# Performance work log

Measured on AMD Instinct MI355X. Metric: run time of the kernel, lower is better.

Reference implementation:

```python
import jax, jax.numpy as jnp
import numpy as np
from jax import lax

# 4D convolution: XLA's general conv supports 4 spatial dims directly.
# dim numbers: N C + 4 spatial (H1 W1 H2 W2)
_DN = ('NCHWDT', 'OIHWDT', 'NCHWDT')


def conv4d(x, w, b):
    # x: [B, Cin, H1, W1, H2, W2]; w: [Cout, Cin, 3,3,3,3]; b: [Cout]
    y = lax.conv_general_dilated(x, w, window_strides=(1, 1, 1, 1),
                                 padding=[(1, 1)] * 4,
                                 dimension_numbers=_DN)
    return y + b.reshape(1, -1, 1, 1, 1, 1)


def setup_inputs() -> dict:
    key = jax.random.key(0)
    ks = jax.random.split(key, 7)
    B, S = 2, 30
    x = jax.random.normal(ks[0], (B, 1, S, S, S, S), dtype=jnp.float32)
    # Conv4d weights, fan-in scaled (kernel 3^4 = 81)
    w1 = jax.random.normal(ks[1], (10, 1, 3, 3, 3, 3), dtype=jnp.float32) * (1.0 / np.sqrt(1 * 81))
    b1 = jax.random.normal(ks[2], (10,), dtype=jnp.float32) * 0.01
    w2 = jax.random.normal(ks[3], (10, 10, 3, 3, 3, 3), dtype=jnp.float32) * (1.0 / np.sqrt(10 * 81))
    b2 = jax.random.normal(ks[4], (10,), dtype=jnp.float32) * 0.01
    w3 = jax.random.normal(ks[5], (1, 10, 3, 3, 3, 3), dtype=jnp.float32) * (1.0 / np.sqrt(10 * 81))
    b3 = jax.random.normal(ks[6], (1,), dtype=jnp.float32) * 0.01
    return {"x": x, "w1": w1, "b1": b1, "w2": w2, "b2": b2, "w3": w3, "b3": b3}


def reference(x, w1, b1, w2, b2, w3, b3):
    def net(t):
        for w, b in ((w1, b1), (w2, b2), (w3, b3)):
            t = jax.nn.relu(conv4d(t, w, b))
        return t

    # symmetric mode: f(x) + permute(f(permute(x)))
    perm = (0, 1, 4, 5, 2, 3)
    return net(x) + jnp.transpose(net(jnp.transpose(x, perm)), perm)
```

## Files before the change

### kernel.cpp

```cpp
#include <hip/hip_runtime.h>


static constexpr int S  = 30;
static constexpr long S4 = 810000;
static constexpr size_t PLANE = 32768;
static constexpr size_t YBYTES = (size_t)1800 * PLANE;

typedef __bf16 bf16x8 __attribute__((ext_vector_type(8)));
typedef float  f32x16 __attribute__((ext_vector_type(16)));
typedef unsigned int  u32;
typedef unsigned short u16;

static __device__ __forceinline__ u16 f2bf(float f) {
    u32 u = __builtin_bit_cast(u32, f);
    return (u16)((u + 0x7fffu + ((u >> 16) & 1u)) >> 16);
}

__global__ __launch_bounds__(256) void fragprep_k(u32* __restrict__ ft,
    const float* __restrict__ w1, const float* __restrict__ w2,
    const float* __restrict__ w3)
{
    const int gid = blockIdx.x * 256 + threadIdx.x;
    if (gid >= 6 * 27 * 64 + 2 * 3 * 64) return;
    const int lane = gid & 63;
    const int n = lane & 31, hl = lane >> 5;
    u16 us[8];
#pragma unroll
    for (int j = 0; j < 8; ++j) us[j] = 0;

    if (gid < 6 * 27 * 64) {
        int r = gid >> 6;
        const int k3 = r % 3; r /= 3;
        const int k12 = r % 9; const int set = r / 9;
        const int layer = set >> 1, swap = set & 1;
        const int k1 = k12 / 3, k2 = k12 % 3;
        if (n < 30) {
            const int k4 = (n < 10) ? 0 : ((n < 20) ? 1 : 2);
            const int co = n - 10 * k4;
            const int i1 = swap ? k3 : k1, i2 = swap ? k4 : k2;
            const int i3 = swap ? k1 : k3, i4 = swap ? k2 : k4;
            const int widx = ((i1 * 3 + i2) * 3 + i3) * 3 + i4;
#pragma unroll
            for (int j = 0; j < 8; ++j) {
                const int k = hl * 8 + j;
                float wv = 0.f;
                if (layer == 0) { if (k == 0) wv = w1[co * 81 + widx]; }
                else if (layer == 1) { if (k < 10) wv = w2[(co * 10 + k) * 81 + widx]; }
                else { if (k < 10 && co == 0) wv = w3[k * 81 + widx]; }
                us[j] = f2bf(wv);
            }
        }
    } else {
        const int idx = gid - 6 * 27 * 64;
        int r = idx >> 6;
        const int k3 = r % 3, swap = r / 3;
        if (n < 30) {
            const int k4 = (n < 10) ? 0 : ((n < 20) ? 1 : 2);
            const int co = n - 10 * k4;
#pragma unroll
            for (int j = 0; j < 8; ++j) {
                const int k12 = hl * 8 + j;
                if (k12 < 9) {
                    const int k1 = k12 / 3, k2 = k12 % 3;
                    const int i1 = swap ? k3 : k1, i2 = swap ? k4 : k2;
                    const int i3 = swap ? k1 : k3, i4 = swap ? k2 : k4;
                    const int widx = ((i1 * 3 + i2) * 3 + i3) * 3 + i4;
                    us[j] = f2bf(w1[co * 81 + widx]);
                }
            }
        }
    }
    u32* o = ft + (size_t)gid * 4;
    o[0] = (u32)us[0] | ((u32)us[1] << 16);
    o[1] = (u32)us[2] | ((u32)us[3] << 16);
    o[2] = (u32)us[4] | ((u32)us[5] << 16);
    o[3] = (u32)us[6] | ((u32)us[7] << 16);
}

__global__ __launch_bounds__(128) void zerok(u16* __restrict__ y1, u16* __restrict__ y2)
{
    const int pb = blockIdx.x, tid = threadIdx.x;
    if (tid >= 124) return;
    int hp, tp;
    if (tid < 32)      { hp = 0;        tp = tid; }
    else if (tid < 64) { hp = 31;       tp = tid - 32; }
    else if (tid < 94) { hp = tid - 63; tp = 0; }
    else               { hp = tid - 93; tp = 31; }
    const size_t off = (size_t)pb * PLANE + hp * 1024 + tp * 32;
    const uint4 z = make_uint4(0, 0, 0, 0);
    *(uint4*)((char*)y1 + off)      = z;
    *(uint4*)((char*)y1 + off + 16) = z;
    *(uint4*)((char*)y2 + off)      = z;
    *(uint4*)((char*)y2 + off + 16) = z;
}

__global__ __launch_bounds__(256, 4) void conv0_k(
    const float* __restrict__ x, const uint4* __restrict__ bt,
    const float* __restrict__ bias, void* __restrict__ outp)
{
    __shared__ float E[4][1056];
    const int wgid = blockIdx.x + S * blockIdx.y + 900 * blockIdx.z;
    const int id2  = (wgid & 7) * 450 + (wgid >> 3);
    const int half = id2 & 1;
    int sp = id2 >> 1;
    const int w1i = sp % S; sp /= S;
    const int h1  = sp % S;
    const int b   = sp / S;

    const int tid = threadIdx.x;
    const int lane = tid & 63, wv = tid >> 6;
    const int m = lane & 31, hl = lane >> 5;
    const int rbase = half * 15 + wv * 4;

    uint4 Bs[3];
#pragma unroll
    for (int ss = 0; ss < 3; ++ss) Bs[ss] = bt[ss * 64 + lane];

    int gof[9]; int gokm = 0;
#pragma unroll
    for (int k12 = 0; k12 < 9; ++k12) {
        const int g1 = h1 + k12 / 3 - 1, g2 = w1i + k12 % 3 - 1;
        gof[k12] = 0;
        if (g1 >= 0 && g1 < S && g2 >= 0 && g2 < S) {
            gof[k12] = (g1 * S + g2) * 900; gokm |= 1 << k12;
        }
    }
    const float* xb = x + (size_t)b * S4;

    uint4 F[6];
#pragma unroll
    for (int f = 0; f < 6; ++f) {
        const int hp = rbase + f;
        const bool rk = (hp >= 1 && hp <= 30 && m >= 1 && m <= 30);
        const int ro = (hp - 1) * 30 + (m - 1);
        u16 av[8];
#pragma unroll
        for (int j = 0; j < 8; ++j) av[j] = 0;
        if (hl == 0) {
#pragma unroll
            for (int j = 0; j < 8; ++j) {
                float v = 0.f;
                if (rk && ((gokm >> j) & 1)) v = xb[gof[j] + ro];
                av[j] = f2bf(v);
            }
        } else {
            float v = 0.f;
            if (rk && ((gokm >> 8) & 1)) v = xb[gof[8] + ro];
            av[0] = f2bf(v);
        }
        F[f] = make_uint4((u32)av[0] | ((u32)av[1] << 16),
                          (u32)av[2] | ((u32)av[3] << 16),
                          (u32)av[4] | ((u32)av[5] << 16),
                          (u32)av[6] | ((u32)av[7] << 16));
    }

    f32x16 acc[4];
#pragma unroll
    for (int r = 0; r < 4; ++r)
#pragma unroll
        for (int e = 0; e < 16; ++e) acc[r][e] = 0.f;
#pragma unroll
    for (int ss = 0; ss < 3; ++ss)
#pragma unroll
        for (int r = 0; r < 4; ++r)
            acc[r] = __builtin_amdgcn_mfma_f32_32x32x16_bf16(
                __builtin_bit_cast(bf16x8, F[r + ss]),
                __builtin_bit_cast(bf16x8, Bs[ss]), acc[r], 0, 0, 0);

    float* Ew = E[wv];
    for (int r = 0; r < 4; ++r) {
        if (wv == 3 && r == 3) continue;
#pragma unroll
        for (int gq = 0; gq < 4; ++gq)
#pragma unroll
            for (int r4 = 0; r4 < 4; ++r4)
                Ew[m * 33 + 4 * hl + 8 * gq + r4] = acc[r][gq * 4 + r4];

        const int h2 = rbase + r;
        char* pl = (char*)outp + ((size_t)b * 900 + h1 * S + w1i) * PLANE
                   + (size_t)(h2 + 1) * 1024;
        const int t = lane >> 1, h8 = lane & 1;
        if (t < 30) {
            u32 wo[4];
#pragma unroll
            for (int p = 0; p < 4; ++p) {
                const int c0 = 8 * h8 + 2 * p, c1 = c0 + 1;
                float v0 = 0.f, v1 = 0.f;
                if (c0 < 10)
                    v0 = fmaxf(Ew[c0 * 33 + t] + Ew[(10 + c0) * 33 + t + 1]
                             + Ew[(20 + c0) * 33 + t + 2] + bias[c0], 0.f);
                if (c1 < 10)
                    v1 = fmaxf(Ew[c1 * 33 + t] + Ew[(10 + c1) * 33 + t + 1]
                             + Ew[(20 + c1) * 33 + t + 2] + bias[c1], 0.f);
                wo[p] = (u32)f2bf(v0) | ((u32)f2bf(v1) << 16);
            }
            *(uint4*)(pl + (t + 1) * 32 + h8 * 16) =
                make_uint4(wo[0], wo[1], wo[2], wo[3]);
        }
    }
}

template<int LAYER, bool ACCUM>
__global__ __launch_bounds__(256, 4) void conv_k(
    const void* __restrict__ inp, const u32* __restrict__ ftab,
    const float* __restrict__ bias, void* __restrict__ outp)
{
    __shared__ float E[4][1056];
    __shared__ uint4 BT[1728];

    const int tid = threadIdx.x;
    {
        const uint4* g = (const uint4*)ftab;
#pragma unroll
        for (int j = 0; j < 7; ++j) {
            const int idx = j * 256 + tid;
            if (idx < 1728) BT[idx] = g[idx];
        }
    }
    __syncthreads();

    const int wgid = blockIdx.x + S * blockIdx.y + 900 * blockIdx.z;
    const int id2  = (wgid & 7) * 450 + (wgid >> 3);
    const int half = id2 & 1;
    int sp = id2 >> 1;
    const int w1i = sp % S; sp /= S;
    const int h1  = sp % S;
    const int b   = sp / S;

    const int lane = tid & 63, wv = tid >> 6;
    const int m = lane & 31, hl = lane >> 5;
    const int rbase = half * 15 + wv * 4;
    const int off5 = (rbase == 27) ? 4096 : 5120;

    int kl[9], nk = 0;
#pragma unroll
    for (int k12 = 0; k12 < 9; ++k12) {
        const int g1 = h1 + k12 / 3 - 1, g2 = w1i + k12 % 3 - 1;
        if (g1 >= 0 && g1 < S && g2 >= 0 && g2 < S)
            kl[nk++] = (g1 * S + g2) | (k12 << 10);
    }

    f32x16 acc[4];
#pragma unroll
    for (int r = 0; r < 4; ++r)
#pragma unroll
        for (int e = 0; e < 16; ++e) acc[r][e] = 0.f;

    const char* Pb = (const char*)inp + (size_t)b * 900 * PLANE
                     + (size_t)rbase * 1024 + m * 32 + hl * 16;

    for (int ki = 0; ki < nk; ++ki) {
        const int g = kl[ki] & 1023, kk = kl[ki] >> 10;
        const char* P = Pb + (size_t)g * PLANE;
        uint4 F[6];
        F[0] = *(const uint4*)(P);
        F[1] = *(const uint4*)(P + 1024);
        F[2] = *(const uint4*)(P + 2048);
        F[3] = *(const uint4*)(P + 3072);
        F[4] = *(const uint4*)(P + 4096);
        F[5] = *(const uint4*)(P + off5);
        uint4 B0[3];
#pragma unroll
        for (int f = 0; f < 3; ++f) B0[f] = BT[(kk * 3 + f) * 64 + lane];

#pragma unroll
        for (int ss = 0; ss < 3; ++ss)
#pragma unroll
            for (int r = 0; r < 4; ++r)
                acc[r] = __builtin_amdgcn_mfma_f32_32x32x16_bf16(
                    __builtin_bit_cast(bf16x8, F[r + ss]),
                    __builtin_bit_cast(bf16x8, B0[ss]), acc[r], 0, 0, 0);
    }

    float* Ew = E[wv];
    for (int r = 0; r < 4; ++r) {
        if (wv == 3 && r == 3) continue;
#pragma unroll
        for (int gq = 0; gq < 4; ++gq)
#pragma unroll
            for (int r4 = 0; r4 < 4; ++r4)
                Ew[m * 33 + 4 * hl + 8 * gq + r4] = acc[r][gq * 4 + r4];

        const int h2 = rbase + r;
        if (LAYER <= 1) {
            char* pl = (char*)outp + ((size_t)b * 900 + h1 * S + w1i) * PLANE
                       + (size_t)(h2 + 1) * 1024;
            const int t = lane >> 1, h8 = lane & 1;
            if (t < 30) {
                u32 wo[4];
#pragma unroll
                for (int p = 0; p < 4; ++p) {
                    const int c0 = 8 * h8 + 2 * p, c1 = c0 + 1;
                    float v0 = 0.f, v1 = 0.f;
                    if (c0 < 10)
                        v0 = fmaxf(Ew[c0 * 33 + t] + Ew[(10 + c0) * 33 + t + 1]
                                 + Ew[(20 + c0) * 33 + t + 2] + bias[c0], 0.f);
                    if (c1 < 10)
                        v1 = fmaxf(Ew[c1 * 33 + t] + Ew[(10 + c1) * 33 + t + 1]
                                 + Ew[(20 + c1) * 33 + t + 2] + bias[c1], 0.f);
                    wo[p] = (u32)f2bf(v0) | ((u32)f2bf(v1) << 16);
                }
                *(uint4*)(pl + (t + 1) * 32 + h8 * 16) =
                    make_uint4(wo[0], wo[1], wo[2], wo[3]);
            }
        } else {
            if (lane < 30) {
                const int t = lane;
                float v = Ew[t] + Ew[330 + t + 1] + Ew[660 + t + 2] + bias[0];
                v = fmaxf(v, 0.f);
                float* o = (float*)outp + (size_t)b * S4
                           + (size_t)(h1 * S + w1i) * 900 + h2 * 30 + t;
                if (ACCUM) *o += v; else *o = v;
            }
        }
    }
}

extern "C" void kernel_launch(void* const* d_in, const int* in_sizes, int n_in,
                              void* d_out, int out_size, void* d_ws, size_t ws_size,
                              hipStream_t stream)
{
    const float* x   = (const float*)d_in[0];
    const float* w1p = (const float*)d_in[1];
    const float* b1p = (const float*)d_in[2];
    const float* w2p = (const float*)d_in[3];
    const float* b2p = (const float*)d_in[4];
    const float* w3p = (const float*)d_in[5];
    const float* b3p = (const float*)d_in[6];
    float* out = (float*)d_out;

    u32* ft = (u32*)d_ws;
    const uint4* ftL0 = (const uint4*)d_ws + 6 * 27 * 64;
    u16* y1 = (u16*)((char*)d_ws + 172032);
    u16* y2 = (u16*)((char*)y1 + YBYTES);

    fragprep_k<<<42, 256, 0, stream>>>(ft, w1p, w2p, w3p);
    zerok<<<1800, 128, 0, stream>>>(y1, y2);

    dim3 grid(S, S, 4), blk(256);
    for (int br = 0; br < 2; ++br) {
        const u32* f2 = ft + (size_t)(2 + br) * 27 * 64 * 4;
        const u32* f3 = ft + (size_t)(4 + br) * 27 * 64 * 4;
        conv0_k<<<grid, blk, 0, stream>>>(x, ftL0 + br * 192, b1p, (void*)y1);
        conv_k<1, false><<<grid, blk, 0, stream>>>(y1, f2, b2p, (void*)y2);
        if (br == 0)
            conv_k<2, false><<<grid, blk, 0, stream>>>(y2, f3, b3p, (void*)out);
        else
            conv_k<2, true><<<grid, blk, 0, stream>>>(y2, f3, b3p, (void*)out);
    }
}
```

Before: 450.2 us.

## Use five waves of three rows and software-prefetch next A tile

The conv kernel now runs 320 threads per block, five waves of three output rows each instead of four waves of four. This removes the special-cased last wave and the odd fifth-row load. The main loop is software-pipelined so the next neighbour plane's A fragments load while the current MFMAs run. The epilogue staging buffer now aliases the weight-table shared memory behind a __syncthreads, which cuts LDS use per block. In exchange, registers per thread rise from the prefetch buffer, and the 5-wave blocks may change how many blocks fit per CU.

Measured after the change: 418.5 us. -7.0%, faster.

```diff
diff --git a/kernel.cpp b/kernel.cpp
--- a/kernel.cpp
+++ b/kernel.cpp
@@ -201,19 +201,19 @@
 }
 
 template<int LAYER, bool ACCUM>
-__global__ __launch_bounds__(256, 4) void conv_k(
+__global__ __launch_bounds__(320, 4) void conv_k(
     const void* __restrict__ inp, const u32* __restrict__ ftab,
     const float* __restrict__ bias, void* __restrict__ outp)
 {
-    __shared__ float E[4][1056];
-    __shared__ uint4 BT[1728];
+    __shared__ char SH[27648];
+    uint4* BT = (uint4*)SH;
 
     const int tid = threadIdx.x;
     {
         const uint4* g = (const uint4*)ftab;
 #pragma unroll
-        for (int j = 0; j < 7; ++j) {
-            const int idx = j * 256 + tid;
+        for (int j = 0; j < 6; ++j) {
+            const int idx = j * 320 + tid;
             if (idx < 1728) BT[idx] = g[idx];
         }
     }
@@ -229,8 +229,7 @@
 
     const int lane = tid & 63, wv = tid >> 6;
     const int m = lane & 31, hl = lane >> 5;
-    const int rbase = half * 15 + wv * 4;
-    const int off5 = (rbase == 27) ? 4096 : 5120;
+    const int rbase = half * 15 + wv * 3;
 
     int kl[9], nk = 0;
 #pragma unroll
@@ -240,41 +239,60 @@
             kl[nk++] = (g1 * S + g2) | (k12 << 10);
     }
 
-    f32x16 acc[4];
-#pragma unroll
-    for (int r = 0; r < 4; ++r)
+    f32x16 acc[3];
+#pragma unroll
+    for (int r = 0; r < 3; ++r)
 #pragma unroll
         for (int e = 0; e < 16; ++e) acc[r][e] = 0.f;
 
     const char* Pb = (const char*)inp + (size_t)b * 900 * PLANE
                      + (size_t)rbase * 1024 + m * 32 + hl * 16;
 
-    for (int ki = 0; ki < nk; ++ki) {
-        const int g = kl[ki] & 1023, kk = kl[ki] >> 10;
+    auto loadA = [&](uint4* Fd, int g) {
         const char* P = Pb + (size_t)g * PLANE;
-        uint4 F[6];
-        F[0] = *(const uint4*)(P);
-        F[1] = *(const uint4*)(P + 1024);
-        F[2] = *(const uint4*)(P + 2048);
-        F[3] = *(const uint4*)(P + 3072);
-        F[4] = *(const uint4*)(P + 4096);
-        F[5] = *(const uint4*)(P + off5);
+        Fd[0] = *(const uint4*)(P);
+        Fd[1] = *(const uint4*)(P + 1024);
+        Fd[2] = *(const uint4*)(P + 2048);
+        Fd[3] = *(const uint4*)(P + 3072);
+        Fd[4] = *(const uint4*)(P + 4096);
+    };
+    auto mfma9 = [&](const uint4* Fs, const uint4* Bs) {
+#pragma unroll
+        for (int ss = 0; ss < 3; ++ss)
+#pragma unroll
+            for (int r = 0; r < 3; ++r)
+                acc[r] = __builtin_amdgcn_mfma_f32_32x32x16_bf16(
+                    __builtin_bit_cast(bf16x8, Fs[r + ss]),
+                    __builtin_bit_cast(bf16x8, Bs[ss]), acc[r], 0, 0, 0);
+    };
+
+    uint4 F[5];
+    loadA(F, kl[0] & 1023);
+
+    for (int ki = 0; ki + 1 < nk; ++ki) {
+        uint4 FN[5];
+        loadA(FN, kl[ki + 1] & 1023);
         uint4 B0[3];
+        {
+            const int kk = kl[ki] >> 10;
+#pragma unroll
+            for (int f = 0; f < 3; ++f) B0[f] = BT[(kk * 3 + f) * 64 + lane];
+        }
+        mfma9(F, B0);
+#pragma unroll
+        for (int f = 0; f < 5; ++f) F[f] = FN[f];
+    }
+    {
+        uint4 B0[3];
+        const int kk = kl[nk - 1] >> 10;
 #pragma unroll
         for (int f = 0; f < 3; ++f) B0[f] = BT[(kk * 3 + f) * 64 + lane];
-
-#pragma unroll
-        for (int ss = 0; ss < 3; ++ss)
-#pragma unroll
-            for (int r = 0; r < 4; ++r)
-                acc[r] = __builtin_amdgcn_mfma_f32_32x32x16_bf16(
-                    __builtin_bit_cast(bf16x8, F[r + ss]),
-                    __builtin_bit_cast(bf16x8, B0[ss]), acc[r], 0, 0, 0);
-    }
-
-    float* Ew = E[wv];
-    for (int r = 0; r < 4; ++r) {
-        if (wv == 3 && r == 3) continue;
+        mfma9(F, B0);
+    }
+
+    __syncthreads();
+    float* Ew = (float*)SH + wv * 1056;
+    for (int r = 0; r < 3; ++r) {
 #pragma unroll
         for (int gq = 0; gq < 4; ++gq)
 #pragma unroll
@@ -337,15 +355,15 @@
     fragprep_k<<<42, 256, 0, stream>>>(ft, w1p, w2p, w3p);
     zerok<<<1800, 128, 0, stream>>>(y1, y2);
 
-    dim3 grid(S, S, 4), blk(256);
+    dim3 grid(S, S, 4);
     for (int br = 0; br < 2; ++br) {
         const u32* f2 = ft + (size_t)(2 + br) * 27 * 64 * 4;
         const u32* f3 = ft + (size_t)(4 + br) * 27 * 64 * 4;
-        conv0_k<<<grid, blk, 0, stream>>>(x, ftL0 + br * 192, b1p, (void*)y1);
-        conv_k<1, false><<<grid, blk, 0, stream>>>(y1, f2, b2p, (void*)y2);
+        conv0_k<<<grid, 256, 0, stream>>>(x, ftL0 + br * 192, b1p, (void*)y1);
+        conv_k<1, false><<<grid, 320, 0, stream>>>(y1, f2, b2p, (void*)y2);
         if (br == 0)
-            conv_k<2, false><<<grid, blk, 0, stream>>>(y2, f3, b3p, (void*)out);
+            conv_k<2, false><<<grid, 320, 0, stream>>>(y2, f3, b3p, (void*)out);
         else
-            conv_k<2, true><<<grid, blk, 0, stream>>>(y2, f3, b3p, (void*)out);
-    }
-}
+            conv_k<2, true><<<grid, 320, 0, stream>>>(y2, f3, b3p, (void*)out);
+    }
+}
```
